# Optimization experiments

Measured on AMD Instinct MI355X. Metric: run time of the kernel, lower is better.

## Reference

```python
import jax, jax.numpy as jnp
import numpy as np

NEG_SLOPE = 0.01  # nn.LeakyReLU default

def leaky_relu(v):
    return jnp.where(v >= 0, v, NEG_SLOPE * v)

def setup_inputs() -> dict:
    key = jax.random.key(0)
    ks = jax.random.split(key, 7)
    B, T, I, H, O = 64, 1024, 512, 1024, 512
    x = jax.random.normal(ks[0], (B, T, I), dtype=jnp.float32)
    # Linear params (stored as [in, out] for x @ W + b)
    W_in = jax.random.normal(ks[1], (I, H), dtype=jnp.float32) * (1.0 / np.sqrt(I))
    b_in = jax.random.normal(ks[2], (H,), dtype=jnp.float32) * 0.01
    W_h = jax.random.normal(ks[3], (2 * H, H), dtype=jnp.float32) * (1.0 / np.sqrt(2 * H))
    b_h = jax.random.normal(ks[4], (H,), dtype=jnp.float32) * 0.01
    W_out = jax.random.normal(ks[5], (H, O), dtype=jnp.float32) * (1.0 / np.sqrt(H))
    b_out = jax.random.normal(ks[6], (O,), dtype=jnp.float32) * 0.01
    return {"x": x, "W_in": W_in, "b_in": b_in, "W_h": W_h, "b_h": b_h,
            "W_out": W_out, "b_out": b_out}

def reference(x, W_in, b_in, W_h, b_h, W_out, b_out):
    B, T, I = x.shape
    H = W_in.shape[1]
    # Precompute input projection for all timesteps in one big GEMM:
    # [B,T,I] @ [I,H] -> [B,T,H], then LeakyReLU.
    h_new_all = leaky_relu(jnp.einsum('bti,ih->bth', x, W_in) + b_in)
    h0 = jnp.zeros((B, H), dtype=x.dtype)

    def step(h, h_new_t):
        combined = jnp.concatenate((h_new_t, h), axis=1)  # [B, 2H]
        h_next = leaky_relu(combined @ W_h + b_h)          # [B, H]
        return h_next, None

    # scan over time axis (sequential dependency on h); dropout_rate=0 => identity
    h_final, _ = jax.lax.scan(step, h0, jnp.swapaxes(h_new_all, 0, 1))
    out = h_final @ W_out + b_out  # [B, O]
    return out
```

## Files before the change

kernel.cpp:

```cpp
#include <hip/hip_runtime.h>
#include <hip/hip_bf16.h>

typedef __attribute__((ext_vector_type(8))) short  s16x8;
typedef __attribute__((ext_vector_type(4))) float  f32x4;
typedef __attribute__((ext_vector_type(4))) unsigned short u16x4;
typedef __attribute__((ext_vector_type(4))) unsigned int   u32x4;

#define B_  64
#define T_  1024
#define I_  512
#define H_  1024
#define O_  512
#define MT_ 65536

#define RG_   8
#define CS_   16

__device__ __forceinline__ unsigned short f2bf(float f) {
    unsigned u = __builtin_bit_cast(unsigned, f);
    u += 0x7FFFu + ((u >> 16) & 1u);
    return (unsigned short)(u >> 16);
}
__device__ __forceinline__ float bf2f(unsigned short h) {
    return __builtin_bit_cast(float, ((unsigned)h) << 16);
}
__device__ __forceinline__ void store_out(float* p, float v) { *p = v; }
__device__ __forceinline__ void store_out(unsigned short* p, float v) { *p = f2bf(v); }
__device__ __forceinline__ void store_nt(float* p, float v) {
    asm volatile("global_store_dword %0, %1, off nt" :: "v"(p), "v"(v) : "memory");
}
__device__ __forceinline__ void store_nt(unsigned short* p, float v) {
    unsigned short h = f2bf(v);
    asm volatile("global_store_short %0, %1, off nt" :: "v"(p), "v"(h) : "memory");
}
__device__ __forceinline__ float to_f32(float v) { return v; }
__device__ __forceinline__ float to_f32(unsigned short v) { return bf2f(v); }

template<typename T> struct pre4;
template<> struct pre4<float>          { using t = f32x4; };
template<> struct pre4<unsigned short> { using t = u16x4; };

__device__ __forceinline__ f32x4 pre_ld(const float* p) {
    f32x4 d; asm volatile("global_load_dwordx4 %0, %1, off nt" : "=v"(d) : "v"(p)); return d;
}
__device__ __forceinline__ u16x4 pre_ld(const unsigned short* p) {
    u16x4 d; asm volatile("global_load_dwordx2 %0, %1, off nt" : "=v"(d) : "v"(p)); return d;
}

#define GL2LDS16(gp, lp) __builtin_amdgcn_global_load_lds( \
    (const __attribute__((address_space(1))) void*)(gp),   \
    (__attribute__((address_space(3))) void*)(lp), 16, 0, 0)

__global__ void cvt_x(const float* __restrict__ src, unsigned short* __restrict__ dst, int n) {
    int stride = gridDim.x * blockDim.x * 4;
    for (int i = (blockIdx.x * blockDim.x + threadIdx.x) * 4; i < n; i += stride) {
        const float4 v = *(const float4*)(src + i);
        u16x4 o;
        o.x = f2bf(v.x); o.y = f2bf(v.y); o.z = f2bf(v.z); o.w = f2bf(v.w);
        *(u16x4*)(dst + i) = o;
    }
}

__global__ void cvt_t(const float* __restrict__ src, unsigned short* __restrict__ dst,
                      int SR, int SC, int row_off) {
    __shared__ unsigned short tile[32][33];
    int c0 = blockIdx.x * 32, r0 = blockIdx.y * 32;
    int tx = threadIdx.x, ty = threadIdx.y;
    #pragma unroll
    for (int i = 0; i < 32; i += 8)
        tile[ty + i][tx] = f2bf(src[(size_t)(row_off + r0 + ty + i) * SC + c0 + tx]);
    __syncthreads();
    #pragma unroll
    for (int i = 0; i < 32; i += 8)
        dst[(size_t)(c0 + ty + i) * SR + r0 + tx] = tile[tx][ty + i];
}

__global__ void strip_h(const unsigned* __restrict__ src, unsigned short* __restrict__ dst) {
    int idx = blockIdx.x * blockDim.x + threadIdx.x;
    u32x4 v = *(const u32x4*)(src + idx * 4);
    int rg = idx >> 11, c2 = idx & 2047;
    int q = c2 >> 9, c3 = c2 & 511;
    int j = c3 >> 6, c = c3 & 63;
    int p = c >> 5, a = (c >> 3) & 3, row = c & 7;
    int grow = rg * 8 + row;
    int col = q * 256 + j * 32 + a * 8 + p * 4;
    u16x4 o;
    o.x = (unsigned short)(v.x >> 16); o.y = (unsigned short)(v.y >> 16);
    o.z = (unsigned short)(v.z >> 16); o.w = (unsigned short)(v.w >> 16);
    *(u16x4*)(dst + (size_t)grow * H_ + col) = o;
}

template<typename OutT, bool LRELU, bool SCATTER>
__global__ __launch_bounds__(256)
void gemm_bf16(const unsigned short* __restrict__ A,
               const unsigned short* __restrict__ BT,
               const float* __restrict__ bias,
               OutT* __restrict__ C, int M, int K, int N)
{
    __shared__ unsigned short As[4096];
    __shared__ unsigned short Bs[4096];
    const int tid = threadIdx.x, lane = tid & 63, wid = tid >> 6;
    const int wr = wid >> 1, wc = wid & 1;
    const int m0 = blockIdx.x * 128, n0 = blockIdx.y * 128;

    f32x4 acc[4][4] = {};

    const int c = wid * 2;
    const int srow = lane >> 2;
    const int scol = (lane & 3) * 8;
    const unsigned short* Ag0 = A  + (size_t)(m0 + c * 16 + srow) * K + scol;
    const unsigned short* Ag1 = A  + (size_t)(m0 + c * 16 + 16 + srow) * K + scol;
    const unsigned short* Bg0 = BT + (size_t)(n0 + c * 16 + srow) * K + scol;
    const unsigned short* Bg1 = BT + (size_t)(n0 + c * 16 + 16 + srow) * K + scol;

    for (int k0 = 0; k0 < K; k0 += 32) {
        __syncthreads();
        GL2LDS16(Ag0 + k0, As + c * 512);
        GL2LDS16(Ag1 + k0, As + (c + 1) * 512);
        GL2LDS16(Bg0 + k0, Bs + c * 512);
        GL2LDS16(Bg1 + k0, Bs + (c + 1) * 512);
        __syncthreads();

        s16x8 af[4], bfr[4];
        #pragma unroll
        for (int i = 0; i < 4; i++)
            af[i] = *(const s16x8*)(As + (wr * 64 + i * 16 + (lane & 15)) * 32 + (lane >> 4) * 8);
        #pragma unroll
        for (int j = 0; j < 4; j++)
            bfr[j] = *(const s16x8*)(Bs + (wc * 64 + j * 16 + (lane & 15)) * 32 + (lane >> 4) * 8);
        #pragma unroll
        for (int i = 0; i < 4; i++)
            #pragma unroll
            for (int j = 0; j < 4; j++)
                acc[i][j] = __builtin_amdgcn_mfma_f32_16x16x32_bf16(af[i], bfr[j], acc[i][j], 0, 0, 0);
    }

    #pragma unroll
    for (int j = 0; j < 4; j++) {
        const int n = n0 + wc * 64 + j * 16 + (lane & 15);
        const float bv = bias[n];
        #pragma unroll
        for (int i = 0; i < 4; i++) {
            #pragma unroll
            for (int r = 0; r < 4; r++) {
                const int m = m0 + wr * 64 + i * 16 + (lane >> 4) * 4 + r;
                if (m < M) {
                    float v = acc[i][j][r] + bv;
                    if (LRELU) v = v >= 0.f ? v : 0.01f * v;
                    if (SCATTER) {
                        size_t row = (size_t)((m & (T_ - 1)) * B_ + (m >> 10));
                        store_nt(&C[row * N + n], v);
                    } else {
                        store_out(&C[(size_t)m * N + n], v);
                    }
                }
            }
        }
    }
}


#define TAGLD2(d, BASE, OFFSTR, SC) asm volatile( \
    "global_load_dwordx4 %0, %1, off offset:" OFFSTR " " SC \
    : "=v"(d) : "v"(BASE))

#define POLLBODY(SC) do { \
    TAGLD2(tv[0],  tA, "0",   SC); TAGLD2(tv[1],  tA, "512",  SC); \
    TAGLD2(tv[2],  tA, "1024",SC); TAGLD2(tv[3],  tA, "1536", SC); \
    TAGLD2(tv[4],  tA, "2048",SC); TAGLD2(tv[5],  tA, "2560", SC); \
    TAGLD2(tv[6],  tA, "3072",SC); TAGLD2(tv[7],  tA, "3584", SC); \
    TAGLD2(tv[8],  tB, "0",   SC); TAGLD2(tv[9],  tB, "512",  SC); \
    TAGLD2(tv[10], tB, "1024",SC); TAGLD2(tv[11], tB, "1536", SC); \
    TAGLD2(tv[12], tB, "2048",SC); TAGLD2(tv[13], tB, "2560", SC); \
    TAGLD2(tv[14], tB, "3072",SC); TAGLD2(tv[15], tB, "3584", SC); \
    } while (0)

#define STEP(S, PVUSE, PVFILL) do { \
    const char* hc32 = (const char*)hbuf32 + (((S) & 1) << 18); \
    char*       hn32 = (char*)hbuf32 + ((((S) + 1) & 1) << 18); \
    const unsigned tagS = (unsigned)(S); \
    const char* tA = hc32 + tbA_off; \
    const char* tB = tA + 4096; \
    for (int i_ = 0; i_ < slp; ++i_) __builtin_amdgcn_s_sleep(2); \
    u32x4 tv[16]; \
    unsigned ok = 0u; \
    int rounds_ = 0; \
    for (;;) { \
        if (!ok) { \
            if (!gmode) { POLLBODY("sc0"); } else { POLLBODY("sc0 sc1"); } \
            asm volatile("s_waitcnt vmcnt(0)" ::: "memory"); \
            __builtin_amdgcn_sched_barrier(0); \
            unsigned d_ = 0; \
            _Pragma("unroll") \
            for (int i = 0; i < 16; i++) \
                d_ |= (tv[i].x ^ tagS) | (tv[i].y ^ tagS) | (tv[i].z ^ tagS) | (tv[i].w ^ tagS); \
            ok = ((d_ & 0xFFFFu) == 0u) ? 1u : 0u; \
        } \
        ++rounds_; \
        if (__all((int)ok)) break; \
        if ((rounds_ & 15) == 0) { \
            unsigned fl; \
            asm volatile("global_load_dword %0, %1, off sc0 sc1\n\t" \
                         "s_waitcnt vmcnt(0)" : "=v"(fl) : "v"(dflag) : "memory"); \
            bool anyfl = __any((int)(fl != 0u)); \
            if (!gmode && (anyfl || rounds_ > 96)) { \
                if (!anyfl && lane == 0) { \
                    unsigned one_ = 1u; \
                    asm volatile("global_store_dword %0, %1, off sc0 sc1" \
                                 :: "v"(dflag), "v"(one_) : "memory"); \
                } \
                gmode = 1u; \
                asm volatile("global_store_dwordx4 %0, %1, off sc0 sc1" \
                             :: "v"(lastsp), "v"(lastow) : "memory"); \
            } \
        } \
        __builtin_amdgcn_s_sleep(1); \
    } \
    slp = (rounds_ > 1) ? (slp + 4 > 24 ? 24 : slp + 4) : (slp > 0 ? slp - 1 : 0); \
    { const int sn = ((S) + 1 < T_) ? (S) + 1 : (S); \
      PVFILL = pre_ld(pre + ((size_t)sn * B_ + hrow) * H_ + col0); } \
    f32x4 ac[4] = {}; \
    _Pragma("unroll") \
    for (int cg = 0; cg < 4; ++cg) { \
        const char* pE = wE + cg * 32768; \
        const char* pO = wO + cg * 32768; \
        _Pragma("unroll") \
        for (int j = 0; j < 8; ++j) { \
            u32x4 a2_ = tv[2 * j], b2_ = tv[2 * j + 1]; \
            u32x4 f_; \
            f_.x = (a2_.x >> 16) | (a2_.y & 0xFFFF0000u); \
            f_.y = (a2_.z >> 16) | (a2_.w & 0xFFFF0000u); \
            f_.z = (b2_.x >> 16) | (b2_.y & 0xFFFF0000u); \
            f_.w = (b2_.z >> 16) | (b2_.w & 0xFFFF0000u); \
            s16x8 hfrag = __builtin_bit_cast(s16x8, f_); \
            s16x8 g = *(const s16x8*)(((j & 1) ? pO : pE) + j * 64); \
            ac[cg] = __builtin_amdgcn_mfma_f32_16x16x32_bf16(g, hfrag, ac[cg], 0, 0, 0); \
        } \
    } \
    if (l15 < 8) { \
        float* pw_ = pbuf + (w * 8 + l15) * 68 + l4 * 4; \
        *(f32x4*)(pw_ +  0) = ac[0]; \
        *(f32x4*)(pw_ + 16) = ac[1]; \
        *(f32x4*)(pw_ + 32) = ac[2]; \
        *(f32x4*)(pw_ + 48) = ac[3]; \
    } \
    asm volatile("s_waitcnt lgkmcnt(0)" ::: "memory"); \
    __builtin_amdgcn_s_barrier(); \
    asm volatile("" ::: "memory"); \
    if (l15 < 8) { \
        const float* pr_ = pbuf + l15 * 68 + w * 16 + l4 * 4; \
        f32x4 s0 = *(const f32x4*)(pr_); \
        f32x4 s1 = *(const f32x4*)(pr_ + 544); \
        f32x4 s2 = *(const f32x4*)(pr_ + 1088); \
        f32x4 s3 = *(const f32x4*)(pr_ + 1632); \
        f32x4 sm = (s0 + s1) + (s2 + s3); \
        u32x4 ow; \
        _Pragma("unroll") \
        for (int r = 0; r < 4; r++) { \
            float v = sm[r] + to_f32(PVUSE[r]); \
            v = v >= 0.f ? v : 0.01f * v; \
            ow[r] = ((unsigned)f2bf(v) << 16) | (tagS + 1u); \
        } \
        char* sp = hn32 + sp_off; \
        if (!gmode) { \
            asm volatile("global_store_dwordx4 %0, %1, off sc0" \
                         :: "v"(sp), "v"(ow) : "memory"); \
        } else { \
            asm volatile("global_store_dwordx4 %0, %1, off sc0 sc1" \
                         :: "v"(sp), "v"(ow) : "memory"); \
        } \
        lastow = ow; lastsp = sp; \
    } \
    asm volatile("s_barrier" ::: "memory"); \
  } while (0)

template<typename PreT>
__global__ __launch_bounds__(256, 1)
void rnn_scan15(const unsigned short* __restrict__ WbotT,
                const PreT* __restrict__ pre,
                unsigned* __restrict__ hbuf32,
                unsigned* __restrict__ dflag)
{
    using p4_t = typename pre4<PreT>::t;
    __shared__ unsigned short Ws[64 * 1024];
    __shared__ float pbuf[4 * 8 * 68];
    const int tid = threadIdx.x, lane = tid & 63, w = tid >> 6;
    const int rg = (int)blockIdx.x & 7;
    const int cs = (int)blockIdx.x >> 3;
    const int n0 = cs * 64;

    for (int idx = tid; idx < 64 * 128; idx += 256) {
        int r = idx >> 7, kb = (idx & 127) * 16;
        s16x8 v = *(const s16x8*)(WbotT + (size_t)(n0 + r) * H_ + (idx & 127) * 8);
        *(s16x8*)((char*)Ws + r * 2048 + (kb ^ ((r & 7) << 4))) = v;
    }
    __syncthreads();

    const int l15 = lane & 15, l4 = lane >> 4;
    const int hrow = rg * 8 + (l15 & 7);
    const int col0 = n0 + w * 16 + l4 * 4;

    const int tbA_off = rg * 32768 + w * 8192 + (lane >> 4) * 128 + (lane & 7) * 16;
    const int q_ = col0 >> 8, j_ = (col0 >> 5) & 7, a_ = (col0 >> 3) & 3, p_ = (col0 >> 2) & 1;
    const int sp_off = rg * 32768 + q_ * 8192 + j_ * 1024 + p_ * 512 + (a_ * 8 + (l15 & 7)) * 16;

    const int b6 = (l15 >> 2) & 1;
    const char* wsRow = (const char*)Ws + l15 * 2048 + ((l4 * 16) ^ ((l15 & 3) << 4)) + w * 512;
    const char* wE = wsRow + b6 * 64;
    const char* wO = wsRow - b6 * 64;

    int slp = 0;
    unsigned gmode = 0;
    u32x4 lastow = {};
    char* lastsp = (char*)dflag + 1024 + tid * 16;

    p4_t pvA, pvB;
    pvA = pre_ld(pre + (size_t)hrow * H_ + col0);
    asm volatile("s_waitcnt vmcnt(0)" ::: "memory");

    for (int t = 0; t < T_; t += 2) {
        STEP(t,     pvA, pvB);
        STEP(t + 1, pvB, pvA);
    }
}

extern "C" void kernel_launch(void* const* d_in, const int* in_sizes, int n_in,
                              void* d_out, int out_size, void* d_ws, size_t ws_size,
                              hipStream_t stream)
{
    const float* x     = (const float*)d_in[0];
    const float* W_in  = (const float*)d_in[1];
    const float* b_in  = (const float*)d_in[2];
    const float* W_h   = (const float*)d_in[3];
    const float* b_h   = (const float*)d_in[4];
    const float* W_out = (const float*)d_in[5];
    const float* b_out = (const float*)d_in[6];
    float* out = (float*)d_out;

    char* ws = (char*)d_ws;
    size_t off = 0;
    auto alloc = [&](size_t bytes) { void* p = ws + off; off += (bytes + 255) & ~(size_t)255; return p; };

    unsigned short* Xb    = (unsigned short*)alloc((size_t)MT_ * I_ * 2);
    unsigned short* WinT  = (unsigned short*)alloc((size_t)H_ * I_ * 2);
    unsigned short* WtopT = (unsigned short*)alloc((size_t)H_ * H_ * 2);
    unsigned short* WbotT = (unsigned short*)alloc((size_t)H_ * H_ * 2);
    unsigned short* WoutT = (unsigned short*)alloc((size_t)O_ * H_ * 2);
    unsigned short* Abuf  = (unsigned short*)alloc((size_t)MT_ * H_ * 2);
    unsigned*       hbuf32 = (unsigned*)alloc((size_t)2 * B_ * H_ * 4);
    unsigned*       dbuf  = (unsigned*)alloc(8192);
    unsigned short* hfin  = (unsigned short*)alloc((size_t)B_ * H_ * 2);
    void* pre = ws + off;
    const bool pre_f32 = (off + (size_t)MT_ * H_ * 4) <= ws_size;

    hipMemsetAsync(hbuf32, 0, (size_t)2 * B_ * H_ * 4, stream);
    hipMemsetAsync(dbuf, 0, 8192, stream);

    cvt_x<<<2048, 256, 0, stream>>>(x, Xb, MT_ * I_);
    dim3 tb(32, 8);
    cvt_t<<<dim3(H_ / 32, I_ / 32), tb, 0, stream>>>(W_in,  WinT,  I_, H_, 0);
    cvt_t<<<dim3(H_ / 32, H_ / 32), tb, 0, stream>>>(W_h,   WtopT, H_, H_, 0);
    cvt_t<<<dim3(H_ / 32, H_ / 32), tb, 0, stream>>>(W_h,   WbotT, H_, H_, H_);
    cvt_t<<<dim3(O_ / 32, H_ / 32), tb, 0, stream>>>(W_out, WoutT, H_, O_, 0);

    gemm_bf16<unsigned short, true, false>
        <<<dim3(MT_ / 128, H_ / 128), 256, 0, stream>>>(Xb, WinT, b_in, Abuf, MT_, I_, H_);

    if (pre_f32) {
        gemm_bf16<float, false, true>
            <<<dim3(MT_ / 128, H_ / 128), 256, 0, stream>>>(Abuf, WtopT, b_h, (float*)pre, MT_, H_, H_);
        rnn_scan15<float><<<RG_ * CS_, 256, 0, stream>>>(WbotT, (const float*)pre, hbuf32, dbuf);
    } else {
        gemm_bf16<unsigned short, false, true>
            <<<dim3(MT_ / 128, H_ / 128), 256, 0, stream>>>(Abuf, WtopT, b_h, (unsigned short*)pre, MT_, H_, H_);
        rnn_scan15<unsigned short><<<RG_ * CS_, 256, 0, stream>>>(WbotT, (const unsigned short*)pre, hbuf32, dbuf);
    }

    strip_h<<<64, 256, 0, stream>>>(hbuf32, hfin);
    gemm_bf16<float, false, false>
        <<<dim3(1, O_ / 128), 256, 0, stream>>>(hfin, WoutT, b_out, out, B_, H_, O_);
}
```

Before: 2.882 ms.

## Give each wave full-K output columns and pipeline polled h loads with MFMAs

Changes the work split in the recurrent scan so each wave computes 16 output columns over the full K=1024 instead of a quarter of K for all 64 columns. This removes the LDS partial-sum reduction and both block barriers per step. The tagged h loads are split into four quarters issued ahead of time, and the wave waits for and validates each quarter with partial vmcnt waits, so global loads overlap the MFMAs. The adaptive sleep now only backs off on stale reads and is capped lower. The cost is that every wave must read the whole h vector, which quadruples polling traffic per block.

```diff
diff --git a/kernel.cpp b/kernel.cpp
--- a/kernel.cpp
+++ b/kernel.cpp
@@ -164,96 +164,112 @@
     "global_load_dwordx4 %0, %1, off offset:" OFFSTR " " SC \
     : "=v"(d) : "v"(BASE))
 
-#define POLLBODY(SC) do { \
-    TAGLD2(tv[0],  tA, "0",   SC); TAGLD2(tv[1],  tA, "512",  SC); \
-    TAGLD2(tv[2],  tA, "1024",SC); TAGLD2(tv[3],  tA, "1536", SC); \
-    TAGLD2(tv[4],  tA, "2048",SC); TAGLD2(tv[5],  tA, "2560", SC); \
-    TAGLD2(tv[6],  tA, "3072",SC); TAGLD2(tv[7],  tA, "3584", SC); \
-    TAGLD2(tv[8],  tB, "0",   SC); TAGLD2(tv[9],  tB, "512",  SC); \
-    TAGLD2(tv[10], tB, "1024",SC); TAGLD2(tv[11], tB, "1536", SC); \
-    TAGLD2(tv[12], tB, "2048",SC); TAGLD2(tv[13], tB, "2560", SC); \
-    TAGLD2(tv[14], tB, "3072",SC); TAGLD2(tv[15], tB, "3584", SC); \
+#define POLLQ(TV, BASE, BASEH, SC) do { \
+    TAGLD2(TV[0],  BASE,  "0",   SC); TAGLD2(TV[1],  BASE,  "512",  SC); \
+    TAGLD2(TV[2],  BASE,  "1024",SC); TAGLD2(TV[3],  BASE,  "1536", SC); \
+    TAGLD2(TV[4],  BASE,  "2048",SC); TAGLD2(TV[5],  BASE,  "2560", SC); \
+    TAGLD2(TV[6],  BASE,  "3072",SC); TAGLD2(TV[7],  BASE,  "3584", SC); \
+    TAGLD2(TV[8],  BASEH, "0",   SC); TAGLD2(TV[9],  BASEH, "512",  SC); \
+    TAGLD2(TV[10], BASEH, "1024",SC); TAGLD2(TV[11], BASEH, "1536", SC); \
+    TAGLD2(TV[12], BASEH, "2048",SC); TAGLD2(TV[13], BASEH, "2560", SC); \
+    TAGLD2(TV[14], BASEH, "3072",SC); TAGLD2(TV[15], BASEH, "3584", SC); \
     } while (0)
+
+#define TAGCHECK(TV, DST) do { \
+    DST = 0; \
+    _Pragma("unroll") \
+    for (int i2_ = 0; i2_ < 16; i2_++) \
+        DST |= (TV[i2_].x ^ tagS) | (TV[i2_].y ^ tagS) | (TV[i2_].z ^ tagS) | (TV[i2_].w ^ tagS); \
+    } while (0)
+
+#define VALQ(TV, BASE, BASEH) do { \
+    unsigned d_; TAGCHECK(TV, d_); \
+    unsigned ok_ = ((d_ & 0xFFFFu) == 0u) ? 1u : 0u; \
+    if (!__all((int)ok_)) { \
+        stale_ = 1u; \
+        int rounds_ = 0; \
+        for (;;) { \
+            if (!ok_) { \
+                if (!gmode) { POLLQ(TV, BASE, BASEH, "sc0"); } \
+                else        { POLLQ(TV, BASE, BASEH, "sc0 sc1"); } \
+                asm volatile("s_waitcnt vmcnt(0)" ::: "memory"); \
+                __builtin_amdgcn_sched_barrier(0); \
+                TAGCHECK(TV, d_); \
+                ok_ = ((d_ & 0xFFFFu) == 0u) ? 1u : 0u; \
+            } \
+            ++rounds_; \
+            if (__all((int)ok_)) break; \
+            if ((rounds_ & 15) == 0) { \
+                unsigned fl; \
+                asm volatile("global_load_dword %0, %1, off sc0 sc1\n\t" \
+                             "s_waitcnt vmcnt(0)" : "=v"(fl) : "v"(dflag) : "memory"); \
+                bool anyfl = __any((int)(fl != 0u)); \
+                if (!gmode && (anyfl || rounds_ > 96)) { \
+                    if (!anyfl && lane == 0) { \
+                        unsigned one_ = 1u; \
+                        asm volatile("global_store_dword %0, %1, off sc0 sc1" \
+                                     :: "v"(dflag), "v"(one_) : "memory"); \
+                    } \
+                    gmode = 1u; \
+                    asm volatile("global_store_dwordx4 %0, %1, off sc0 sc1" \
+                                 :: "v"(lastsp), "v"(lastow) : "memory"); \
+                } \
+            } \
+            __builtin_amdgcn_s_sleep(1); \
+        } \
+    } } while (0)
+
+#define MFMA8(TV, J0) do { \
+    _Pragma("unroll") \
+    for (int j3_ = 0; j3_ < 8; ++j3_) { \
+        const int jj_ = (J0) + j3_; \
+        u32x4 a2_ = TV[2 * j3_], b2_ = TV[2 * j3_ + 1]; \
+        u32x4 f_; \
+        f_.x = (a2_.x >> 16) | (a2_.y & 0xFFFF0000u); \
+        f_.y = (a2_.z >> 16) | (a2_.w & 0xFFFF0000u); \
+        f_.z = (b2_.x >> 16) | (b2_.y & 0xFFFF0000u); \
+        f_.w = (b2_.z >> 16) | (b2_.w & 0xFFFF0000u); \
+        s16x8 hfrag = __builtin_bit_cast(s16x8, f_); \
+        s16x8 g = *(const s16x8*)(((jj_ & 1) ? pO : pE) + jj_ * 64); \
+        ac[jj_ & 3] = __builtin_amdgcn_mfma_f32_16x16x32_bf16(g, hfrag, ac[jj_ & 3], 0, 0, 0); \
+    } } while (0)
+
+#define WAITN(NSTR) do { \
+    asm volatile("s_waitcnt vmcnt(" NSTR ")" ::: "memory"); \
+    __builtin_amdgcn_sched_barrier(0); } while (0)
 
 #define STEP(S, PVUSE, PVFILL) do { \
     const char* hc32 = (const char*)hbuf32 + (((S) & 1) << 18); \
     char*       hn32 = (char*)hbuf32 + ((((S) + 1) & 1) << 18); \
     const unsigned tagS = (unsigned)(S); \
-    const char* tA = hc32 + tbA_off; \
-    const char* tB = tA + 4096; \
+    const char* b0 = hc32 + qoff;       const char* b0h = b0 + 4096; \
+    const char* b1 = b0 + 8192;         const char* b1h = b1 + 4096; \
+    const char* b2 = b0 + 16384;        const char* b2h = b2 + 4096; \
+    const char* b3 = b0 + 24576;        const char* b3h = b3 + 4096; \
+    unsigned stale_ = 0u; \
     for (int i_ = 0; i_ < slp; ++i_) __builtin_amdgcn_s_sleep(2); \
-    u32x4 tv[16]; \
-    unsigned ok = 0u; \
-    int rounds_ = 0; \
-    for (;;) { \
-        if (!ok) { \
-            if (!gmode) { POLLBODY("sc0"); } else { POLLBODY("sc0 sc1"); } \
-            asm volatile("s_waitcnt vmcnt(0)" ::: "memory"); \
-            __builtin_amdgcn_sched_barrier(0); \
-            unsigned d_ = 0; \
-            _Pragma("unroll") \
-            for (int i = 0; i < 16; i++) \
-                d_ |= (tv[i].x ^ tagS) | (tv[i].y ^ tagS) | (tv[i].z ^ tagS) | (tv[i].w ^ tagS); \
-            ok = ((d_ & 0xFFFFu) == 0u) ? 1u : 0u; \
-        } \
-        ++rounds_; \
-        if (__all((int)ok)) break; \
-        if ((rounds_ & 15) == 0) { \
-            unsigned fl; \
-            asm volatile("global_load_dword %0, %1, off sc0 sc1\n\t" \
-                         "s_waitcnt vmcnt(0)" : "=v"(fl) : "v"(dflag) : "memory"); \
-            bool anyfl = __any((int)(fl != 0u)); \
-            if (!gmode && (anyfl || rounds_ > 96)) { \
-                if (!anyfl && lane == 0) { \
-                    unsigned one_ = 1u; \
-                    asm volatile("global_store_dword %0, %1, off sc0 sc1" \
-                                 :: "v"(dflag), "v"(one_) : "memory"); \
-                } \
-                gmode = 1u; \
-                asm volatile("global_store_dwordx4 %0, %1, off sc0 sc1" \
-                             :: "v"(lastsp), "v"(lastow) : "memory"); \
-            } \
-        } \
-        __builtin_amdgcn_s_sleep(1); \
-    } \
-    slp = (rounds_ > 1) ? (slp + 4 > 24 ? 24 : slp + 4) : (slp > 0 ? slp - 1 : 0); \
+    u32x4 tv0[16], tv1[16]; \
+    f32x4 ac[4] = {}; \
+    if (!gmode) { POLLQ(tv0, b0, b0h, "sc0"); POLLQ(tv1, b1, b1h, "sc0"); } \
+    else        { POLLQ(tv0, b0, b0h, "sc0 sc1"); POLLQ(tv1, b1, b1h, "sc0 sc1"); } \
+    WAITN("16"); \
+    VALQ(tv0, b0, b0h); \
+    MFMA8(tv0, 0); \
+    if (!gmode) { POLLQ(tv0, b2, b2h, "sc0"); } else { POLLQ(tv0, b2, b2h, "sc0 sc1"); } \
+    WAITN("16"); \
+    VALQ(tv1, b1, b1h); \
+    MFMA8(tv1, 8); \
+    if (!gmode) { POLLQ(tv1, b3, b3h, "sc0"); } else { POLLQ(tv1, b3, b3h, "sc0 sc1"); } \
     { const int sn = ((S) + 1 < T_) ? (S) + 1 : (S); \
       PVFILL = pre_ld(pre + ((size_t)sn * B_ + hrow) * H_ + col0); } \
-    f32x4 ac[4] = {}; \
-    _Pragma("unroll") \
-    for (int cg = 0; cg < 4; ++cg) { \
-        const char* pE = wE + cg * 32768; \
-        const char* pO = wO + cg * 32768; \
-        _Pragma("unroll") \
-        for (int j = 0; j < 8; ++j) { \
-            u32x4 a2_ = tv[2 * j], b2_ = tv[2 * j + 1]; \
-            u32x4 f_; \
-            f_.x = (a2_.x >> 16) | (a2_.y & 0xFFFF0000u); \
-            f_.y = (a2_.z >> 16) | (a2_.w & 0xFFFF0000u); \
-            f_.z = (b2_.x >> 16) | (b2_.y & 0xFFFF0000u); \
-            f_.w = (b2_.z >> 16) | (b2_.w & 0xFFFF0000u); \
-            s16x8 hfrag = __builtin_bit_cast(s16x8, f_); \
-            s16x8 g = *(const s16x8*)(((j & 1) ? pO : pE) + j * 64); \
-            ac[cg] = __builtin_amdgcn_mfma_f32_16x16x32_bf16(g, hfrag, ac[cg], 0, 0, 0); \
-        } \
-    } \
+    WAITN("17"); \
+    VALQ(tv0, b2, b2h); \
+    MFMA8(tv0, 16); \
+    WAITN("0"); \
+    VALQ(tv1, b3, b3h); \
+    MFMA8(tv1, 24); \
+    f32x4 sm = (ac[0] + ac[1]) + (ac[2] + ac[3]); \
     if (l15 < 8) { \
-        float* pw_ = pbuf + (w * 8 + l15) * 68 + l4 * 4; \
-        *(f32x4*)(pw_ +  0) = ac[0]; \
-        *(f32x4*)(pw_ + 16) = ac[1]; \
-        *(f32x4*)(pw_ + 32) = ac[2]; \
-        *(f32x4*)(pw_ + 48) = ac[3]; \
-    } \
-    asm volatile("s_waitcnt lgkmcnt(0)" ::: "memory"); \
-    __builtin_amdgcn_s_barrier(); \
-    asm volatile("" ::: "memory"); \
-    if (l15 < 8) { \
-        const float* pr_ = pbuf + l15 * 68 + w * 16 + l4 * 4; \
-        f32x4 s0 = *(const f32x4*)(pr_); \
-        f32x4 s1 = *(const f32x4*)(pr_ + 544); \
-        f32x4 s2 = *(const f32x4*)(pr_ + 1088); \
-        f32x4 s3 = *(const f32x4*)(pr_ + 1632); \
-        f32x4 sm = (s0 + s1) + (s2 + s3); \
         u32x4 ow; \
         _Pragma("unroll") \
         for (int r = 0; r < 4; r++) { \
@@ -271,19 +287,18 @@
         } \
         lastow = ow; lastsp = sp; \
     } \
-    asm volatile("s_barrier" ::: "memory"); \
+    slp = stale_ ? (slp + 2 > 8 ? 8 : slp + 2) : (slp > 0 ? slp - 1 : 0); \
   } while (0)
 
 template<typename PreT>
 __global__ __launch_bounds__(256, 1)
-void rnn_scan15(const unsigned short* __restrict__ WbotT,
+void rnn_scan17(const unsigned short* __restrict__ WbotT,
                 const PreT* __restrict__ pre,
                 unsigned* __restrict__ hbuf32,
                 unsigned* __restrict__ dflag)
 {
     using p4_t = typename pre4<PreT>::t;
     __shared__ unsigned short Ws[64 * 1024];
-    __shared__ float pbuf[4 * 8 * 68];
     const int tid = threadIdx.x, lane = tid & 63, w = tid >> 6;
     const int rg = (int)blockIdx.x & 7;
     const int cs = (int)blockIdx.x >> 3;
@@ -300,14 +315,15 @@
     const int hrow = rg * 8 + (l15 & 7);
     const int col0 = n0 + w * 16 + l4 * 4;
 
-    const int tbA_off = rg * 32768 + w * 8192 + (lane >> 4) * 128 + (lane & 7) * 16;
+    const int qoff = rg * 32768 + l4 * 128 + (lane & 7) * 16;
     const int q_ = col0 >> 8, j_ = (col0 >> 5) & 7, a_ = (col0 >> 3) & 3, p_ = (col0 >> 2) & 1;
     const int sp_off = rg * 32768 + q_ * 8192 + j_ * 1024 + p_ * 512 + (a_ * 8 + (l15 & 7)) * 16;
 
     const int b6 = (l15 >> 2) & 1;
-    const char* wsRow = (const char*)Ws + l15 * 2048 + ((l4 * 16) ^ ((l15 & 3) << 4)) + w * 512;
-    const char* wE = wsRow + b6 * 64;
-    const char* wO = wsRow - b6 * 64;
+    const char* wsRowF = (const char*)Ws + (size_t)(w * 16 + l15) * 2048
+                       + ((l4 * 16) ^ ((l15 & 3) << 4));
+    const char* pE = wsRowF + b6 * 64;
+    const char* pO = wsRowF - b6 * 64;
 
     int slp = 0;
     unsigned gmode = 0;
@@ -369,11 +385,11 @@
     if (pre_f32) {
         gemm_bf16<float, false, true>
             <<<dim3(MT_ / 128, H_ / 128), 256, 0, stream>>>(Abuf, WtopT, b_h, (float*)pre, MT_, H_, H_);
-        rnn_scan15<float><<<RG_ * CS_, 256, 0, stream>>>(WbotT, (const float*)pre, hbuf32, dbuf);
+        rnn_scan17<float><<<RG_ * CS_, 256, 0, stream>>>(WbotT, (const float*)pre, hbuf32, dbuf);
     } else {
         gemm_bf16<unsigned short, false, true>
             <<<dim3(MT_ / 128, H_ / 128), 256, 0, stream>>>(Abuf, WtopT, b_h, (unsigned short*)pre, MT_, H_, H_);
-        rnn_scan15<unsigned short><<<RG_ * CS_, 256, 0, stream>>>(WbotT, (const unsigned short*)pre, hbuf32, dbuf);
+        rnn_scan17<unsigned short><<<RG_ * CS_, 256, 0, stream>>>(WbotT, (const unsigned short*)pre, hbuf32, dbuf);
     }
 
     strip_h<<<64, 256, 0, stream>>>(hbuf32, hfin);
```

Result: slower. 4.990 ms (+73.2%).
